# Kernel optimization log

Measured on AMD Instinct MI355X. Metric: run time of the kernel, lower is better.

The kernel has to match this reference:

```python
import jax, jax.numpy as jnp
import numpy as np

LN_EPS = 1e-5
NEG_INF = -1e30


def setup_inputs() -> dict:
    key = jax.random.key(0)
    ks = jax.random.split(key, 8)
    B, S, D_MODEL, Q_IN = 1, 2048, 1024, 512
    HI, DI = 16, 64            # indexer heads / head_dim
    H, DQK, DV = 8, 64, 64     # MLA heads, qk_head_dim, v_head_dim
    return {
        "x": jax.random.normal(ks[0], (B, S, D_MODEL), jnp.float32),
        "q_input": jax.random.normal(ks[1], (B, S, Q_IN), jnp.float32),
        "q": jax.random.normal(ks[2], (B, S, H, DQK), jnp.float32),
        "k": jax.random.normal(ks[3], (B, S, H, DQK), jnp.float32),
        "v": jax.random.normal(ks[4], (B, S, H, DV), jnp.float32),
        "w_q": jax.random.normal(ks[5], (Q_IN, HI * DI), jnp.float32) * (Q_IN ** -0.5),
        "w_k": jax.random.normal(ks[6], (D_MODEL, DI), jnp.float32) * (D_MODEL ** -0.5),
        "ln_g": jnp.ones((DI,), jnp.float32),
        "ln_b": jnp.zeros((DI,), jnp.float32),
        "w_weights": jax.random.normal(ks[7], (D_MODEL, HI), jnp.float32) * (D_MODEL ** -0.5),
        "top_k": 128,
    }


def _indexer_topk(x, q_input, w_q, w_k, ln_g, ln_b, w_weights, top_k):
    """Lightning indexer: per-head relevance scores -> weighted sum -> causal top-k indices."""
    B, S, _ = x.shape
    HI = w_weights.shape[1]
    DI = w_k.shape[1]
    qi = (q_input @ w_q).reshape(B, S, HI, DI)          # bqhd
    ki = x @ w_k                                         # bkd
    mu = ki.mean(-1, keepdims=True)
    var = ((ki - mu) ** 2).mean(-1, keepdims=True)
    ki = (ki - mu) * jax.lax.rsqrt(var + LN_EPS) * ln_g + ln_b
    # per-head weights; scores*w summed over h == (sum_h w*q) . k  (fused, same math)
    w = (x @ w_weights) * (HI ** -0.5)                   # bqh
    q_eff = jnp.einsum("bqhd,bqh->bqd", qi, w) * (DI ** -0.5)
    scores = jnp.einsum("bqd,bkd->bqk", q_eff, ki)       # [B,S,S]
    pos = jnp.arange(S)
    causal = jnp.where(pos[None, :] <= pos[:, None], 0.0, NEG_INF).astype(scores.dtype)
    scores = scores + causal[None]
    return jax.lax.top_k(scores, top_k)[1]               # [B,S,K]


def reference(x, q_input, q, k, v, w_q, w_k, ln_g, ln_b, w_weights, top_k):
    B, S, H, DQK = q.shape
    DV = v.shape[-1]
    idx = _indexer_topk(x, q_input, w_q, w_k, ln_g, ln_b, w_weights, top_k)  # [B,S,K]

    qh = q.transpose(0, 2, 1, 3)   # [B,H,Sq,D]
    kh = k.transpose(0, 2, 1, 3)   # [B,H,Sk,D]
    vh = v.transpose(0, 2, 1, 3)

    def gather(kv, ix):            # kv [Sk,D], ix [Sq,K] -> [Sq,K,D]
        return kv[ix]

    gather_h = jax.vmap(gather, in_axes=(0, None))       # over heads, shared idx
    gather_bh = jax.vmap(gather_h, in_axes=(0, 0))       # over batch
    k_sel = gather_bh(kh, idx)     # [B,H,Sq,K,D]
    v_sel = gather_bh(vh, idx)     # [B,H,Sq,K,Dv]

    att = jnp.einsum("bhqd,bhqkd->bhqk", qh, k_sel) * (DQK ** -0.5)
    pos = jnp.arange(S)
    valid = idx[:, None, :, :] <= pos[None, None, :, None]   # causal validity of gathered idx
    att = jnp.where(valid, att, NEG_INF)
    p = jax.nn.softmax(att, axis=-1)
    out = jnp.einsum("bhqk,bhqkd->bhqd", p, v_sel)
    return out.transpose(0, 2, 1, 3)   # [B,S,H,Dv]
```

## Files before the change

### kernel.cpp

```cpp
#include <hip/hip_runtime.h>
#include <hip/hip_bf16.h>
#include <hip/hip_fp16.h>
#include <math.h>

#define S 2048
#define DM 1024
#define QIN 512
#define HI 16
#define DI 64
#define NH 8
#define TOPK 128
#define LN_EPS 1e-5f
#define KP 16
#define KVSZ (S * NH * 64)

typedef float f32x4 __attribute__((ext_vector_type(4)));
typedef short s16x8 __attribute__((ext_vector_type(8)));

__device__ __forceinline__ float wave_sum(float v){
#pragma unroll
  for (int o = 32; o; o >>= 1) v += __shfl_xor(v, o);
  return v;
}
__device__ __forceinline__ float wave_max(float v){
#pragma unroll
  for (int o = 32; o; o >>= 1) v = fmaxf(v, __shfl_xor(v, o));
  return v;
}
__device__ __forceinline__ unsigned short f2bf(float x){
  unsigned u = __float_as_uint(x);
  unsigned r = u + 0x7FFFu + ((u >> 16) & 1u);
  return (unsigned short)(r >> 16);
}
__device__ __forceinline__ float bf2f(unsigned short s){
  return __uint_as_float(((unsigned)s) << 16);
}
__device__ __forceinline__ unsigned short f2h(float x){
  return __half_as_ushort(__float2half_rn(x));
}
union UH2 { unsigned int u; __half2 h; };
__device__ __forceinline__ __half2 as_half2(unsigned int u){ UH2 x; x.u = u; return x.h; }

#define MFMA3(ACC, AH, AL, BH, BL) \
  ACC = __builtin_amdgcn_mfma_f32_16x16x32_bf16(AH, BH, ACC, 0, 0, 0); \
  ACC = __builtin_amdgcn_mfma_f32_16x16x32_bf16(AH, BL, ACC, 0, 0, 0); \
  ACC = __builtin_amdgcn_mfma_f32_16x16x32_bf16(AL, BH, ACC, 0, 0, 0);

#define MFMA6(ACC, AH, AM, AL, BH, BM, BL) \
  ACC = __builtin_amdgcn_mfma_f32_16x16x32_bf16(AH, BH, ACC, 0, 0, 0); \
  ACC = __builtin_amdgcn_mfma_f32_16x16x32_bf16(AH, BM, ACC, 0, 0, 0); \
  ACC = __builtin_amdgcn_mfma_f32_16x16x32_bf16(AM, BH, ACC, 0, 0, 0); \
  ACC = __builtin_amdgcn_mfma_f32_16x16x32_bf16(AH, BL, ACC, 0, 0, 0); \
  ACC = __builtin_amdgcn_mfma_f32_16x16x32_bf16(AL, BH, ACC, 0, 0, 0); \
  ACC = __builtin_amdgcn_mfma_f32_16x16x32_bf16(AM, BM, ACC, 0, 0, 0);

__global__ __launch_bounds__(256) void k_f1(const float* __restrict__ x,
                                            const float* __restrict__ wk,
                                            const float* __restrict__ ww,
                                            float* __restrict__ part,
                                            const float* __restrict__ qin,
                                            unsigned short* __restrict__ Ah,
                                            unsigned short* __restrict__ Al,
                                            const float* __restrict__ k,
                                            unsigned short* __restrict__ kh,
                                            const float* __restrict__ v,
                                            unsigned short* __restrict__ vh,
                                            const float* __restrict__ wq,
                                            unsigned short* __restrict__ Bh,
                                            unsigned short* __restrict__ Bl){
  __shared__ float As[32][68];
  __shared__ float Bs[32][84];
  const int bid = blockIdx.x;
  const int t = threadIdx.x;

  if (bid < 512){
    const int kp = bid & 15;
    const int bm = bid >> 4;
    const int m0 = bm * 64;
    const int tm = (t & 15) * 4;
    const int tn = (t >> 4) * 5;
    float acc[4][5];
#pragma unroll
    for (int i = 0; i < 4; i++)
#pragma unroll
      for (int j = 0; j < 5; j++) acc[i][j] = 0.f;

    for (int kb = 0; kb < (DM / KP) / 32; ++kb){
      const int k0 = kp * (DM / KP) + kb * 32;
#pragma unroll
      for (int i = 0; i < 2; i++){
        int u = t + i * 256;
        int m = u >> 3, c4 = u & 7;
        float4 a = *(const float4*)&x[(size_t)(m0 + m) * DM + k0 + c4 * 4];
        As[c4*4+0][m] = a.x; As[c4*4+1][m] = a.y; As[c4*4+2][m] = a.z; As[c4*4+3][m] = a.w;
      }
#pragma unroll
      for (int i = 0; i < 10; i++){
        int u = t + i * 256;
        int kk = u / 80, nn = u % 80;
        float val = (nn < 64) ? wk[(size_t)(k0 + kk) * 64 + nn]
                              : ww[(size_t)(k0 + kk) * 16 + (nn - 64)];
        Bs[kk][nn] = val;
      }
      __syncthreads();
#pragma unroll
      for (int kk = 0; kk < 32; ++kk){
        float4 a = *(const float4*)&As[kk][tm];
        float av[4] = {a.x, a.y, a.z, a.w};
        float bb[5];
#pragma unroll
        for (int j = 0; j < 5; j++) bb[j] = Bs[kk][tn + j];
#pragma unroll
        for (int i = 0; i < 4; i++)
#pragma unroll
          for (int j = 0; j < 5; j++) acc[i][j] = fmaf(av[i], bb[j], acc[i][j]);
      }
      __syncthreads();
    }
    float* dst = part + (size_t)kp * S * 80;
#pragma unroll
    for (int i = 0; i < 4; i++)
#pragma unroll
      for (int j = 0; j < 5; j++)
        dst[(size_t)(m0 + tm + i) * 80 + tn + j] = acc[i][j];
    return;
  }

  if (bid < 512 + 3072){
    const int SEG0 = S * QIN / 4;
    const int SEG1 = KVSZ / 4;
    int id = (bid - 512) * 256 + t;
    if (id < SEG0){
      float4 f = ((const float4*)qin)[id];
      ushort4 h, lo;
      h.x = f2bf(f.x); lo.x = f2bf(f.x - bf2f(h.x));
      h.y = f2bf(f.y); lo.y = f2bf(f.y - bf2f(h.y));
      h.z = f2bf(f.z); lo.z = f2bf(f.z - bf2f(h.z));
      h.w = f2bf(f.w); lo.w = f2bf(f.w - bf2f(h.w));
      ((ushort4*)Ah)[id] = h;
      ((ushort4*)Al)[id] = lo;
    } else if (id < SEG0 + SEG1){
      int j = id - SEG0;
      float4 f = ((const float4*)k)[j];
      ushort4 o;
      o.x = f2h(f.x); o.y = f2h(f.y); o.z = f2h(f.z); o.w = f2h(f.w);
      ((ushort4*)kh)[j] = o;
    } else {
      int j = id - SEG0 - SEG1;
      float4 f = ((const float4*)v)[j];
      ushort4 o;
      o.x = f2h(f.x); o.y = f2h(f.y); o.z = f2h(f.z); o.w = f2h(f.w);
      ((ushort4*)vh)[j] = o;
    }
    return;
  }

  {
    unsigned short (*lh)[33] = (unsigned short(*)[33])&As[0][0];
    unsigned short (*ll)[33] = (unsigned short(*)[33])&Bs[0][0];
    const int b2 = bid - 3584;
    const int k0 = (b2 & 15) * 32;
    const int n0 = (b2 >> 4) * 32;
    const int c = t & 31, r8 = t >> 5;
#pragma unroll
    for (int i = 0; i < 4; ++i){
      int kk = r8 + i * 8;
      float wv = wq[(size_t)(k0 + kk) * 1024 + n0 + c];
      unsigned short h = f2bf(wv);
      lh[c][kk] = h;
      ll[c][kk] = f2bf(wv - bf2f(h));
    }
    __syncthreads();
    const int kk = t & 31, nl = t >> 5;
#pragma unroll
    for (int i = 0; i < 4; ++i){
      int nn = nl + i * 8;
      Bh[(size_t)(n0 + nn) * QIN + k0 + kk] = lh[nn][kk];
      Bl[(size_t)(n0 + nn) * QIN + k0 + kk] = ll[nn][kk];
    }
  }
}

__global__ __launch_bounds__(256) void k_f2(const float* __restrict__ part,
                                            const float* __restrict__ g,
                                            const float* __restrict__ b,
                                            unsigned short* __restrict__ kih,
                                            unsigned short* __restrict__ kim,
                                            unsigned short* __restrict__ kil,
                                            float* __restrict__ wgt,
                                            const unsigned short* __restrict__ Ah,
                                            const unsigned short* __restrict__ Al,
                                            const unsigned short* __restrict__ Bh,
                                            const unsigned short* __restrict__ Bl,
                                            float* __restrict__ qi){
  __shared__ short Ash[64][72];
  __shared__ short Asl[64][72];
  __shared__ short Bsh[64][72];
  __shared__ short Bsl[64][72];
  const int bid = blockIdx.x;
  const int t = threadIdx.x;
  if (bid < 512){
    const int s = bid * 4 + (t >> 6);
    const int l = t & 63;
    float kv = 0.f;
#pragma unroll
    for (int p = 0; p < KP; p++) kv += part[(size_t)p * S * 80 + (size_t)s * 80 + l];
    float wv = 0.f;
    if (l < 16){
#pragma unroll
      for (int p = 0; p < KP; p++) wv += part[(size_t)p * S * 80 + (size_t)s * 80 + 64 + l];
    }
    float mu = wave_sum(kv) * (1.f / 64.f);
    float d  = kv - mu;
    float var = wave_sum(d * d) * (1.f / 64.f);
    float o = d * (1.f / sqrtf(var + LN_EPS)) * g[l] + b[l];
    unsigned short h = f2bf(o);
    float r1 = o - bf2f(h);
    unsigned short m = f2bf(r1);
    kih[(size_t)s * 64 + l] = h;
    kim[(size_t)s * 64 + l] = m;
    kil[(size_t)s * 64 + l] = f2bf(r1 - bf2f(m));
    if (l < 16) wgt[(size_t)s * 16 + l] = wv * 0.25f;
    return;
  }
  const int b2 = bid - 512;
  const int bn = b2 & 15;
  const int bm = b2 >> 4;
  const int w = t >> 6, l = t & 63;
  const int r = l & 15, kg = l >> 4;
  const int m0 = bm * 64 + (w >> 1) * 32;
  const int n0 = bn * 64 + (w & 1) * 32;
  const int mq = (w >> 1) * 32;
  const int nq = (w & 1) * 32;
  const int srow = t >> 3;
  const int scol = (t & 7) * 8;

  f32x4 acc00 = {0,0,0,0}, acc01 = {0,0,0,0}, acc10 = {0,0,0,0}, acc11 = {0,0,0,0};

  for (int kb = 0; kb < QIN / 64; ++kb){
    const int k0 = kb * 64;
#pragma unroll
    for (int i = 0; i < 2; ++i){
      int row = srow + i * 32;
      size_t ga = (size_t)(bm * 64 + row) * QIN + k0 + scol;
      size_t gb = (size_t)(bn * 64 + row) * QIN + k0 + scol;
      *(s16x8*)&Ash[row][scol] = *(const s16x8*)(Ah + ga);
      *(s16x8*)&Asl[row][scol] = *(const s16x8*)(Al + ga);
      *(s16x8*)&Bsh[row][scol] = *(const s16x8*)(Bh + gb);
      *(s16x8*)&Bsl[row][scol] = *(const s16x8*)(Bl + gb);
    }
    __syncthreads();
#pragma unroll
    for (int ks = 0; ks < 2; ++ks){
      const int ko = ks * 32 + kg * 8;
      s16x8 ah0 = *(const s16x8*)&Ash[mq + r][ko];
      s16x8 ah1 = *(const s16x8*)&Ash[mq + 16 + r][ko];
      s16x8 al0 = *(const s16x8*)&Asl[mq + r][ko];
      s16x8 al1 = *(const s16x8*)&Asl[mq + 16 + r][ko];
      s16x8 bh0 = *(const s16x8*)&Bsh[nq + r][ko];
      s16x8 bh1 = *(const s16x8*)&Bsh[nq + 16 + r][ko];
      s16x8 bl0 = *(const s16x8*)&Bsl[nq + r][ko];
      s16x8 bl1 = *(const s16x8*)&Bsl[nq + 16 + r][ko];
      MFMA3(acc00, ah0, al0, bh0, bl0)
      MFMA3(acc01, ah0, al0, bh1, bl1)
      MFMA3(acc10, ah1, al1, bh0, bl0)
      MFMA3(acc11, ah1, al1, bh1, bl1)
    }
    __syncthreads();
  }
#pragma unroll
  for (int j = 0; j < 4; ++j){
    qi[(size_t)(m0 +  0 + kg * 4 + j) * 1024 + n0 +  0 + r] = acc00[j];
    qi[(size_t)(m0 +  0 + kg * 4 + j) * 1024 + n0 + 16 + r] = acc01[j];
    qi[(size_t)(m0 + 16 + kg * 4 + j) * 1024 + n0 +  0 + r] = acc10[j];
    qi[(size_t)(m0 + 16 + kg * 4 + j) * 1024 + n0 + 16 + r] = acc11[j];
  }
}

__global__ __launch_bounds__(256) void k_f3(const float* __restrict__ qi,
                                            const float* __restrict__ wgt,
                                            unsigned short* __restrict__ qeh,
                                            unsigned short* __restrict__ qem,
                                            unsigned short* __restrict__ qel){
  const int id = blockIdx.x * 256 + threadIdx.x;
  const int s = id >> 6, d = id & 63;
  float acc = 0.f;
#pragma unroll
  for (int h = 0; h < 16; h++)
    acc = fmaf(wgt[(size_t)s * 16 + h], qi[(size_t)s * 1024 + h * 64 + d], acc);
  acc *= 0.125f;
  unsigned short hh = f2bf(acc);
  float r1 = acc - bf2f(hh);
  unsigned short mm = f2bf(r1);
  qeh[(size_t)s * 64 + d] = hh;
  qem[(size_t)s * 64 + d] = mm;
  qel[(size_t)s * 64 + d] = f2bf(r1 - bf2f(mm));
}

__global__ __launch_bounds__(256) void k_scores(const unsigned short* __restrict__ qeh,
                                                const unsigned short* __restrict__ qem,
                                                const unsigned short* __restrict__ qel,
                                                const unsigned short* __restrict__ kih,
                                                const unsigned short* __restrict__ kim,
                                                const unsigned short* __restrict__ kil,
                                                float* __restrict__ sc){
  const int bj = blockIdx.x, bi = blockIdx.y;
  if (bj > bi) return;
  const int w = threadIdx.x >> 6, l = threadIdx.x & 63;
  const int r = l & 15, kg = l >> 4;
  const int m0 = bi * 64 + (w >> 1) * 32;
  const int n0 = bj * 64 + (w & 1) * 32;
  f32x4 acc00 = {0,0,0,0}, acc01 = {0,0,0,0}, acc10 = {0,0,0,0}, acc11 = {0,0,0,0};
  const size_t aoff = (size_t)(m0 + r) * 64 + kg * 8;
  const size_t boff = (size_t)(n0 + r) * 64 + kg * 8;
#pragma unroll
  for (int k0 = 0; k0 < 64; k0 += 32){
    s16x8 ah0 = *(const s16x8*)(qeh + aoff + k0);
    s16x8 ah1 = *(const s16x8*)(qeh + aoff + 16 * 64 + k0);
    s16x8 am0 = *(const s16x8*)(qem + aoff + k0);
    s16x8 am1 = *(const s16x8*)(qem + aoff + 16 * 64 + k0);
    s16x8 al0 = *(const s16x8*)(qel + aoff + k0);
    s16x8 al1 = *(const s16x8*)(qel + aoff + 16 * 64 + k0);
    s16x8 bh0 = *(const s16x8*)(kih + boff + k0);
    s16x8 bh1 = *(const s16x8*)(kih + boff + 16 * 64 + k0);
    s16x8 bm0 = *(const s16x8*)(kim + boff + k0);
    s16x8 bm1 = *(const s16x8*)(kim + boff + 16 * 64 + k0);
    s16x8 bl0 = *(const s16x8*)(kil + boff + k0);
    s16x8 bl1 = *(const s16x8*)(kil + boff + 16 * 64 + k0);
    MFMA6(acc00, ah0, am0, al0, bh0, bm0, bl0)
    MFMA6(acc01, ah0, am0, al0, bh1, bm1, bl1)
    MFMA6(acc10, ah1, am1, al1, bh0, bm0, bl0)
    MFMA6(acc11, ah1, am1, al1, bh1, bm1, bl1)
  }
#pragma unroll
  for (int j = 0; j < 4; ++j){
    sc[(size_t)(m0 +  0 + kg * 4 + j) * S + n0 +  0 + r] = acc00[j];
    sc[(size_t)(m0 +  0 + kg * 4 + j) * S + n0 + 16 + r] = acc01[j];
    sc[(size_t)(m0 + 16 + kg * 4 + j) * S + n0 +  0 + r] = acc10[j];
    sc[(size_t)(m0 + 16 + kg * 4 + j) * S + n0 + 16 + r] = acc11[j];
  }
}

__global__ __launch_bounds__(256) void k_ta(const float* __restrict__ sc,
                                            const float* __restrict__ q,
                                            const unsigned short* __restrict__ kh,
                                            const unsigned short* __restrict__ vh,
                                            float* __restrict__ out){
  const int i = blockIdx.x, t = threadIdx.x;
  const int w = t >> 6, l = t & 63;
  const int ncand = i + 1;

  __shared__ unsigned int keys[S];
  __shared__ int lA[S];
  __shared__ int lB[S];
  __shared__ int hist[256];
  __shared__ int wtot[4];
  __shared__ int sres[TOPK];
  __shared__ int s_b, s_above, s_out, s_m;
  __shared__ float sp[4][2][TOPK];

  if (ncand <= TOPK){
    if (t < TOPK) sres[t] = (t < ncand) ? t : 0;
    __syncthreads();
  } else {
    hist[t] = 0;
    if (t == 0) s_out = 0;
    __syncthreads();
    for (int j = t; j < ncand; j += 256){
      unsigned int u = __float_as_uint(sc[(size_t)i * S + j]);
      unsigned int kk = (u & 0x80000000u) ? ~u : (u | 0x80000000u);
      keys[j] = kk;
      atomicAdd(&hist[kk >> 24], 1);
    }
    __syncthreads();
    int rem = TOPK;
    {
      const int h = hist[t];
      int vsc = h;
#pragma unroll
      for (int off = 1; off < 64; off <<= 1){
        int u = __shfl_down(vsc, off);
        if (l + off < 64) vsc += u;
      }
      if (l == 0) wtot[w] = vsc;
      __syncthreads();
      int later = 0;
#pragma unroll
      for (int ww = 1; ww < 4; ++ww) if (ww > w) later += wtot[ww];
      const int excl = vsc + later - h;
      if (excl < rem && excl + h >= rem){ s_b = t; s_above = excl; }
      __syncthreads();
    }
    int b = s_b;
    rem -= s_above;
    if (t == 0) s_m = 0;
    __syncthreads();
    for (int b0 = 0; b0 < ncand; b0 += 256){
      int j = b0 + t;
      bool valid = j < ncand;
      unsigned int kk = valid ? keys[j] : 0u;
      int by = kk >> 24;
      bool pgt = valid && (by > b);
      bool peq = valid && (by == b);
      unsigned long long mgt = __ballot(pgt);
      unsigned long long meq = __ballot(peq);
      int basegt = 0, baseeq = 0;
      if (l == 0){
        basegt = atomicAdd(&s_out, __popcll(mgt));
        baseeq = atomicAdd(&s_m, __popcll(meq));
      }
      basegt = __shfl(basegt, 0);
      baseeq = __shfl(baseeq, 0);
      unsigned long long lanemask = (1ull << l) - 1ull;
      if (pgt) sres[basegt + __popcll(mgt & lanemask)] = j;
      if (peq) lA[baseeq + __popcll(meq & lanemask)] = j;
    }
    __syncthreads();
    int m = s_m;
    int* Lsrc = lA; int* Ldst = lB;
    bool done = false;
    if (m == rem){
      int base = TOPK - rem;
      for (int u = t; u < m; u += 256) sres[base + u] = Lsrc[u];
      done = true;
    }
    for (int p = 2; p >= 0 && !done; --p){
      const int sh = p * 8;
      __syncthreads();
      hist[t] = 0;
      __syncthreads();
      for (int u = t; u < m; u += 256) atomicAdd(&hist[(keys[Lsrc[u]] >> sh) & 255], 1);
      __syncthreads();
      {
        const int h = hist[t];
        int vsc = h;
#pragma unroll
        for (int off = 1; off < 64; off <<= 1){
          int u = __shfl_down(vsc, off);
          if (l + off < 64) vsc += u;
        }
        if (l == 0) wtot[w] = vsc;
        __syncthreads();
        int later = 0;
#pragma unroll
        for (int ww = 1; ww < 4; ++ww) if (ww > w) later += wtot[ww];
        const int excl = vsc + later - h;
        if (excl < rem && excl + h >= rem){ s_b = t; s_above = excl; }
        __syncthreads();
      }
      b = s_b;
      rem -= s_above;
      if (t == 0) s_m = 0;
      __syncthreads();
      for (int u = t; u < m; u += 256){
        int j = Lsrc[u]; int by = (keys[j] >> sh) & 255;
        if (by > b){ int p2 = atomicAdd(&s_out, 1); sres[p2] = j; }
        else if (by == b){ int p2 = atomicAdd(&s_m, 1); Ldst[p2] = j; }
      }
      __syncthreads();
      m = s_m;
      { int* tmp = Lsrc; Lsrc = Ldst; Ldst = tmp; }
      if (m == rem){
        int base = TOPK - rem;
        for (int u = t; u < m; u += 256) sres[base + u] = Lsrc[u];
        done = true;
      }
    }
    if (!done && t == 0){
      int base = TOPK - rem;
      for (int a = 0; a < rem; ++a){
        int mn = 1 << 30, pos = -1;
        for (int u = 0; u < m; ++u){ int j = Lsrc[u]; if (j < mn){ mn = j; pos = u; } }
        sres[base + a] = mn; Lsrc[pos] = 1 << 30;
      }
    }
    __syncthreads();
  }

  const int n = (ncand < TOPK) ? ncand : TOPK;
  const int h0 = 2 * w, h1 = h0 + 1;
  const int g = l >> 3, gl = l & 7;
  const float* qrow = q + (size_t)i * (NH * 64);
  __half2 qa2[4], qb2[4];
  {
    float4 a0 = *(const float4*)&qrow[h0 * 64 + gl * 8];
    float4 a1 = *(const float4*)&qrow[h0 * 64 + gl * 8 + 4];
    float4 b0 = *(const float4*)&qrow[h1 * 64 + gl * 8];
    float4 b1 = *(const float4*)&qrow[h1 * 64 + gl * 8 + 4];
    qa2[0] = __floats2half2_rn(a0.x * 0.125f, a0.y * 0.125f);
    qa2[1] = __floats2half2_rn(a0.z * 0.125f, a0.w * 0.125f);
    qa2[2] = __floats2half2_rn(a1.x * 0.125f, a1.y * 0.125f);
    qa2[3] = __floats2half2_rn(a1.z * 0.125f, a1.w * 0.125f);
    qb2[0] = __floats2half2_rn(b0.x * 0.125f, b0.y * 0.125f);
    qb2[1] = __floats2half2_rn(b0.z * 0.125f, b0.w * 0.125f);
    qb2[2] = __floats2half2_rn(b1.x * 0.125f, b1.y * 0.125f);
    qb2[3] = __floats2half2_rn(b1.z * 0.125f, b1.w * 0.125f);
  }

#pragma unroll 8
  for (int pass = 0; pass < TOPK / 8; ++pass){
    const int j = pass * 8 + g;
    const int sj = (j < n) ? sres[j] : 0;
    const size_t base = (size_t)sj * (NH * 64);
    uint4 u0 = *(const uint4*)(kh + base + h0 * 64 + gl * 8);
    uint4 u1 = *(const uint4*)(kh + base + h1 * 64 + gl * 8);
    __half2 acc0 = __floats2half2_rn(0.f, 0.f);
    __half2 acc1 = __floats2half2_rn(0.f, 0.f);
    acc0 = __hfma2(as_half2(u0.x), qa2[0], acc0);
    acc0 = __hfma2(as_half2(u0.y), qa2[1], acc0);
    acc0 = __hfma2(as_half2(u0.z), qa2[2], acc0);
    acc0 = __hfma2(as_half2(u0.w), qa2[3], acc0);
    acc1 = __hfma2(as_half2(u1.x), qb2[0], acc1);
    acc1 = __hfma2(as_half2(u1.y), qb2[1], acc1);
    acc1 = __hfma2(as_half2(u1.z), qb2[2], acc1);
    acc1 = __hfma2(as_half2(u1.w), qb2[3], acc1);
    float d0 = __low2float(acc0) + __high2float(acc0);
    float d1 = __low2float(acc1) + __high2float(acc1);
#pragma unroll
    for (int o = 1; o < 8; o <<= 1){ d0 += __shfl_xor(d0, o); d1 += __shfl_xor(d1, o); }
    if (gl == 0){ sp[w][0][j] = d0; sp[w][1][j] = d1; }
  }
  asm volatile("" ::: "memory");

  const bool v0 = (l < n), v1 = (l + 64 < n);
  {
    float s0 = v0 ? sp[w][0][l] : -1e30f, s1 = v1 ? sp[w][0][l + 64] : -1e30f;
    float m = wave_max(fmaxf(s0, s1));
    float e0 = v0 ? __expf(s0 - m) : 0.f;
    float e1 = v1 ? __expf(s1 - m) : 0.f;
    float inv = 1.f / wave_sum(e0 + e1);
    sp[w][0][l] = e0 * inv;
    sp[w][0][l + 64] = e1 * inv;
  }
  {
    float s0 = v0 ? sp[w][1][l] : -1e30f, s1 = v1 ? sp[w][1][l + 64] : -1e30f;
    float m = wave_max(fmaxf(s0, s1));
    float e0 = v0 ? __expf(s0 - m) : 0.f;
    float e1 = v1 ? __expf(s1 - m) : 0.f;
    float inv = 1.f / wave_sum(e0 + e1);
    sp[w][1][l] = e0 * inv;
    sp[w][1][l + 64] = e1 * inv;
  }
  asm volatile("" ::: "memory");

  const int kq = l >> 4;
  const int hp = (l >> 3) & 1;
  const int d8 = (l & 7) * 8;
  float o8[8] = {0,0,0,0,0,0,0,0};
#pragma unroll 8
  for (int pass = 0; pass < TOPK / 4; ++pass){
    const int j = pass * 4 + kq;
    const int sj = (j < n) ? sres[j] : 0;
    const size_t base = (size_t)sj * (NH * 64);
    uint4 uv = *(const uint4*)(vh + base + (h0 + hp) * 64 + d8);
    float p = sp[w][hp][j];
    __half2 va = as_half2(uv.x), vb = as_half2(uv.y), vc = as_half2(uv.z), vd = as_half2(uv.w);
    o8[0] = fmaf(p, __low2float(va),  o8[0]);
    o8[1] = fmaf(p, __high2float(va), o8[1]);
    o8[2] = fmaf(p, __low2float(vb),  o8[2]);
    o8[3] = fmaf(p, __high2float(vb), o8[3]);
    o8[4] = fmaf(p, __low2float(vc),  o8[4]);
    o8[5] = fmaf(p, __high2float(vc), o8[5]);
    o8[6] = fmaf(p, __low2float(vd),  o8[6]);
    o8[7] = fmaf(p, __high2float(vd), o8[7]);
  }
#pragma unroll
  for (int e = 0; e < 8; ++e){
    o8[e] += __shfl_xor(o8[e], 16);
    o8[e] += __shfl_xor(o8[e], 32);
  }
  if (l < 16){
    float* dst = &out[(size_t)i * (NH * 64) + (h0 + hp) * 64 + d8];
    *(float4*)dst       = make_float4(o8[0], o8[1], o8[2], o8[3]);
    *(float4*)(dst + 4) = make_float4(o8[4], o8[5], o8[6], o8[7]);
  }
}

extern "C" void kernel_launch(void* const* d_in, const int* in_sizes, int n_in,
                              void* d_out, int out_size, void* d_ws, size_t ws_size,
                              hipStream_t stream){
  const float* x   = (const float*)d_in[0];
  const float* qin = (const float*)d_in[1];
  const float* q   = (const float*)d_in[2];
  const float* k   = (const float*)d_in[3];
  const float* v   = (const float*)d_in[4];
  const float* wq  = (const float*)d_in[5];
  const float* wk  = (const float*)d_in[6];
  const float* lng = (const float*)d_in[7];
  const float* lnb = (const float*)d_in[8];
  const float* ww  = (const float*)d_in[9];
  float* out = (float*)d_out;

  float* ws = (float*)d_ws;
  float* part = ws;
  float* wgt  = ws + 2621440;
  float* qi   = ws + 2654208;
  float* sc   = ws + 4751360;
  unsigned short* kh  = (unsigned short*)(ws + 8945664);
  unsigned short* vh  = (unsigned short*)(ws + 9469952);
  unsigned short* kih = (unsigned short*)(ws + 9994240);
  unsigned short* kim = (unsigned short*)(ws + 10059776);
  unsigned short* kil = (unsigned short*)(ws + 10125312);
  unsigned short* qeh = (unsigned short*)(ws + 10190848);
  unsigned short* qem = (unsigned short*)(ws + 10256384);
  unsigned short* qel = (unsigned short*)(ws + 10321920);
  unsigned short* Ah  = (unsigned short*)(ws + 10387456);
  unsigned short* Al  = (unsigned short*)(ws + 10911744);
  unsigned short* Bh  = (unsigned short*)(ws + 11436032);
  unsigned short* Bl  = (unsigned short*)(ws + 11698176);

  hipLaunchKernelGGL(k_f1,     dim3(4096),   dim3(256), 0, stream,
                     x, wk, ww, part, qin, Ah, Al, k, kh, v, vh, wq, Bh, Bl);
  hipLaunchKernelGGL(k_f2,     dim3(1024),   dim3(256), 0, stream,
                     part, lng, lnb, kih, kim, kil, wgt, Ah, Al, Bh, Bl, qi);
  hipLaunchKernelGGL(k_f3,     dim3(512),    dim3(256), 0, stream,
                     qi, wgt, qeh, qem, qel);
  hipLaunchKernelGGL(k_scores, dim3(32, 32), dim3(256), 0, stream,
                     qeh, qem, qel, kih, kim, kil, sc);
  hipLaunchKernelGGL(k_ta,     dim3(2048),   dim3(256), 0, stream,
                     sc, q, kh, vh, out);
}
```

Measured before the change: 98.95 us.

## Replace LDS-buffered radix select with prefix-filtered re-reads of score row

```diff
diff --git a/kernel.cpp b/kernel.cpp
--- a/kernel.cpp
+++ b/kernel.cpp
@@ -13,6 +13,7 @@
 #define LN_EPS 1e-5f
 #define KP 16
 #define KVSZ (S * NH * 64)
+#define TBCAP 384
 
 typedef float f32x4 __attribute__((ext_vector_type(4)));
 typedef short s16x8 __attribute__((ext_vector_type(8)));
@@ -37,6 +38,10 @@
 }
 __device__ __forceinline__ unsigned short f2h(float x){
   return __half_as_ushort(__float2half_rn(x));
+}
+__device__ __forceinline__ unsigned int sortkey(float x){
+  unsigned u = __float_as_uint(x);
+  return (u & 0x80000000u) ? ~u : (u | 0x80000000u);
 }
 union UH2 { unsigned int u; __half2 h; };
 __device__ __forceinline__ __half2 as_half2(unsigned int u){ UH2 x; x.u = u; return x.h; }
@@ -350,86 +355,31 @@
   const int w = t >> 6, l = t & 63;
   const int ncand = i + 1;
 
-  __shared__ unsigned int keys[S];
-  __shared__ int lA[S];
-  __shared__ int lB[S];
   __shared__ int hist[256];
   __shared__ int wtot[4];
   __shared__ int sres[TOPK];
+  __shared__ int tb[TBCAP];
   __shared__ int s_b, s_above, s_out, s_m;
   __shared__ float sp[4][2][TOPK];
 
+  const float* srow = sc + (size_t)i * S;
+
   if (ncand <= TOPK){
     if (t < TOPK) sres[t] = (t < ncand) ? t : 0;
     __syncthreads();
   } else {
-    hist[t] = 0;
-    if (t == 0) s_out = 0;
-    __syncthreads();
-    for (int j = t; j < ncand; j += 256){
-      unsigned int u = __float_as_uint(sc[(size_t)i * S + j]);
-      unsigned int kk = (u & 0x80000000u) ? ~u : (u | 0x80000000u);
-      keys[j] = kk;
-      atomicAdd(&hist[kk >> 24], 1);
-    }
-    __syncthreads();
+    unsigned int prefix = 0;
     int rem = TOPK;
-    {
-      const int h = hist[t];
-      int vsc = h;
-#pragma unroll
-      for (int off = 1; off < 64; off <<= 1){
-        int u = __shfl_down(vsc, off);
-        if (l + off < 64) vsc += u;
-      }
-      if (l == 0) wtot[w] = vsc;
-      __syncthreads();
-      int later = 0;
-#pragma unroll
-      for (int ww = 1; ww < 4; ++ww) if (ww > w) later += wtot[ww];
-      const int excl = vsc + later - h;
-      if (excl < rem && excl + h >= rem){ s_b = t; s_above = excl; }
-      __syncthreads();
-    }
-    int b = s_b;
-    rem -= s_above;
-    if (t == 0) s_m = 0;
-    __syncthreads();
-    for (int b0 = 0; b0 < ncand; b0 += 256){
-      int j = b0 + t;
-      bool valid = j < ncand;
-      unsigned int kk = valid ? keys[j] : 0u;
-      int by = kk >> 24;
-      bool pgt = valid && (by > b);
-      bool peq = valid && (by == b);
-      unsigned long long mgt = __ballot(pgt);
-      unsigned long long meq = __ballot(peq);
-      int basegt = 0, baseeq = 0;
-      if (l == 0){
-        basegt = atomicAdd(&s_out, __popcll(mgt));
-        baseeq = atomicAdd(&s_m, __popcll(meq));
-      }
-      basegt = __shfl(basegt, 0);
-      baseeq = __shfl(baseeq, 0);
-      unsigned long long lanemask = (1ull << l) - 1ull;
-      if (pgt) sres[basegt + __popcll(mgt & lanemask)] = j;
-      if (peq) lA[baseeq + __popcll(meq & lanemask)] = j;
-    }
-    __syncthreads();
-    int m = s_m;
-    int* Lsrc = lA; int* Ldst = lB;
-    bool done = false;
-    if (m == rem){
-      int base = TOPK - rem;
-      for (int u = t; u < m; u += 256) sres[base + u] = Lsrc[u];
-      done = true;
-    }
-    for (int p = 2; p >= 0 && !done; --p){
+#pragma unroll
+    for (int p = 3; p >= 0; --p){
       const int sh = p * 8;
-      __syncthreads();
       hist[t] = 0;
       __syncthreads();
-      for (int u = t; u < m; u += 256) atomicAdd(&hist[(keys[Lsrc[u]] >> sh) & 255], 1);
+      const unsigned int himask = (p == 3) ? 0u : (0xFFFFFFFFu << (sh + 8));
+      for (int j = t; j < ncand; j += 256){
+        unsigned int kk = sortkey(srow[j]);
+        if ((kk & himask) == (prefix & himask)) atomicAdd(&hist[(kk >> sh) & 255], 1);
+      }
       __syncthreads();
       {
         const int h = hist[t];
@@ -448,31 +398,41 @@
         if (excl < rem && excl + h >= rem){ s_b = t; s_above = excl; }
         __syncthreads();
       }
-      b = s_b;
+      prefix |= ((unsigned int)s_b) << sh;
       rem -= s_above;
-      if (t == 0) s_m = 0;
-      __syncthreads();
-      for (int u = t; u < m; u += 256){
-        int j = Lsrc[u]; int by = (keys[j] >> sh) & 255;
-        if (by > b){ int p2 = atomicAdd(&s_out, 1); sres[p2] = j; }
-        else if (by == b){ int p2 = atomicAdd(&s_m, 1); Ldst[p2] = j; }
-      }
-      __syncthreads();
-      m = s_m;
-      { int* tmp = Lsrc; Lsrc = Ldst; Ldst = tmp; }
-      if (m == rem){
-        int base = TOPK - rem;
-        for (int u = t; u < m; u += 256) sres[base + u] = Lsrc[u];
-        done = true;
-      }
-    }
-    if (!done && t == 0){
-      int base = TOPK - rem;
-      for (int a = 0; a < rem; ++a){
-        int mn = 1 << 30, pos = -1;
-        for (int u = 0; u < m; ++u){ int j = Lsrc[u]; if (j < mn){ mn = j; pos = u; } }
-        sres[base + a] = mn; Lsrc[pos] = 1 << 30;
-      }
+    }
+    if (t == 0){ s_out = 0; s_m = 0; }
+    __syncthreads();
+    for (int b0 = 0; b0 < ncand; b0 += 256){
+      int j = b0 + t;
+      bool valid = j < ncand;
+      unsigned int kk = valid ? sortkey(srow[j]) : 0u;
+      bool pgt = valid && (kk > prefix);
+      bool peq = valid && (kk == prefix);
+      unsigned long long mgt = __ballot(pgt);
+      unsigned long long meq = __ballot(peq);
+      int basegt = 0, baseeq = 0;
+      if (l == 0){
+        basegt = (mgt ? atomicAdd(&s_out, __popcll(mgt)) : 0);
+        baseeq = (meq ? atomicAdd(&s_m, __popcll(meq)) : 0);
+      }
+      basegt = __shfl(basegt, 0);
+      baseeq = __shfl(baseeq, 0);
+      unsigned long long lanemask = (1ull << l) - 1ull;
+      if (pgt) sres[basegt + __popcll(mgt & lanemask)] = j;
+      if (peq){
+        int p2 = baseeq + __popcll(meq & lanemask);
+        if (p2 < TBCAP) tb[p2] = j;
+      }
+    }
+    __syncthreads();
+    const int nout = s_out;
+    if (s_m == rem){
+      for (int u2 = t; u2 < rem; u2 += 256) sres[nout + u2] = tb[u2];
+    } else if (t == 0){
+      int taken = 0;
+      for (int j = 0; j < ncand && taken < rem; ++j)
+        if (sortkey(srow[j]) == prefix) sres[nout + taken++] = j;
     }
     __syncthreads();
   }
```

Result: slower. 103.0 us (+4.1%).

## Split fused top-k/attention kernel into separate top-k and per-wave attention kernels

Applied to the files above, without the earlier changes.

```diff
diff --git a/kernel.cpp b/kernel.cpp
--- a/kernel.cpp
+++ b/kernel.cpp
@@ -341,39 +341,92 @@
   }
 }
 
-__global__ __launch_bounds__(256) void k_ta(const float* __restrict__ sc,
-                                            const float* __restrict__ q,
-                                            const unsigned short* __restrict__ kh,
-                                            const unsigned short* __restrict__ vh,
-                                            float* __restrict__ out){
+__global__ __launch_bounds__(256) void k_topk(const float* __restrict__ sc,
+                                              int* __restrict__ idx,
+                                              int* __restrict__ cnt){
   const int i = blockIdx.x, t = threadIdx.x;
   const int w = t >> 6, l = t & 63;
-  const int ncand = i + 1;
-
+  const int n = i + 1;
+  int* outr = idx + (size_t)i * TOPK;
+  if (n <= TOPK){
+    for (int m = t; m < n; m += 256) outr[m] = m;
+    if (t == 0) cnt[i] = n;
+    return;
+  }
   __shared__ unsigned int keys[S];
   __shared__ int lA[S];
   __shared__ int lB[S];
   __shared__ int hist[256];
   __shared__ int wtot[4];
-  __shared__ int sres[TOPK];
   __shared__ int s_b, s_above, s_out, s_m;
-  __shared__ float sp[4][2][TOPK];
-
-  if (ncand <= TOPK){
-    if (t < TOPK) sres[t] = (t < ncand) ? t : 0;
-    __syncthreads();
-  } else {
+  hist[t] = 0;
+  if (t == 0) s_out = 0;
+  __syncthreads();
+  for (int j = t; j < n; j += 256){
+    unsigned int u = __float_as_uint(sc[(size_t)i * S + j]);
+    unsigned int kk = (u & 0x80000000u) ? ~u : (u | 0x80000000u);
+    keys[j] = kk;
+    atomicAdd(&hist[kk >> 24], 1);
+  }
+  __syncthreads();
+  int rem = TOPK;
+  {
+    const int h = hist[t];
+    int vsc = h;
+#pragma unroll
+    for (int off = 1; off < 64; off <<= 1){
+      int u = __shfl_down(vsc, off);
+      if (l + off < 64) vsc += u;
+    }
+    if (l == 0) wtot[w] = vsc;
+    __syncthreads();
+    int later = 0;
+#pragma unroll
+    for (int ww = 1; ww < 4; ++ww) if (ww > w) later += wtot[ww];
+    const int excl = vsc + later - h;
+    if (excl < rem && excl + h >= rem){ s_b = t; s_above = excl; }
+    __syncthreads();
+  }
+  int b = s_b;
+  rem -= s_above;
+  if (t == 0) s_m = 0;
+  __syncthreads();
+  for (int b0 = 0; b0 < n; b0 += 256){
+    int j = b0 + t;
+    bool valid = j < n;
+    unsigned int kk = valid ? keys[j] : 0u;
+    int by = kk >> 24;
+    bool pgt = valid && (by > b);
+    bool peq = valid && (by == b);
+    unsigned long long mgt = __ballot(pgt);
+    unsigned long long meq = __ballot(peq);
+    int basegt = 0, baseeq = 0;
+    if (l == 0){
+      basegt = (mgt ? atomicAdd(&s_out, __popcll(mgt)) : 0);
+      baseeq = (meq ? atomicAdd(&s_m, __popcll(meq)) : 0);
+    }
+    basegt = __shfl(basegt, 0);
+    baseeq = __shfl(baseeq, 0);
+    unsigned long long lanemask = (1ull << l) - 1ull;
+    if (pgt) outr[basegt + __popcll(mgt & lanemask)] = j;
+    if (peq) lA[baseeq + __popcll(meq & lanemask)] = j;
+  }
+  __syncthreads();
+  int m = s_m;
+  int* Lsrc = lA; int* Ldst = lB;
+  bool done = false;
+  if (m == rem){
+    int base = TOPK - rem;
+    for (int u = t; u < m; u += 256) outr[base + u] = Lsrc[u];
+    done = true;
+  }
+  for (int p = 2; p >= 0 && !done; --p){
+    const int sh = p * 8;
+    __syncthreads();
     hist[t] = 0;
-    if (t == 0) s_out = 0;
-    __syncthreads();
-    for (int j = t; j < ncand; j += 256){
-      unsigned int u = __float_as_uint(sc[(size_t)i * S + j]);
-      unsigned int kk = (u & 0x80000000u) ? ~u : (u | 0x80000000u);
-      keys[j] = kk;
-      atomicAdd(&hist[kk >> 24], 1);
-    }
-    __syncthreads();
-    int rem = TOPK;
+    __syncthreads();
+    for (int u = t; u < m; u += 256) atomicAdd(&hist[(keys[Lsrc[u]] >> sh) & 255], 1);
+    __syncthreads();
     {
       const int h = hist[t];
       int vsc = h;
@@ -391,93 +444,54 @@
       if (excl < rem && excl + h >= rem){ s_b = t; s_above = excl; }
       __syncthreads();
     }
-    int b = s_b;
+    b = s_b;
     rem -= s_above;
     if (t == 0) s_m = 0;
     __syncthreads();
-    for (int b0 = 0; b0 < ncand; b0 += 256){
-      int j = b0 + t;
-      bool valid = j < ncand;
-      unsigned int kk = valid ? keys[j] : 0u;
-      int by = kk >> 24;
-      bool pgt = valid && (by > b);
-      bool peq = valid && (by == b);
-      unsigned long long mgt = __ballot(pgt);
-      unsigned long long meq = __ballot(peq);
-      int basegt = 0, baseeq = 0;
-      if (l == 0){
-        basegt = atomicAdd(&s_out, __popcll(mgt));
-        baseeq = atomicAdd(&s_m, __popcll(meq));
-      }
-      basegt = __shfl(basegt, 0);
-      baseeq = __shfl(baseeq, 0);
-      unsigned long long lanemask = (1ull << l) - 1ull;
-      if (pgt) sres[basegt + __popcll(mgt & lanemask)] = j;
-      if (peq) lA[baseeq + __popcll(meq & lanemask)] = j;
-    }
-    __syncthreads();
-    int m = s_m;
-    int* Lsrc = lA; int* Ldst = lB;
-    bool done = false;
+    for (int u = t; u < m; u += 256){
+      int j = Lsrc[u]; int by = (keys[j] >> sh) & 255;
+      if (by > b){ int p2 = atomicAdd(&s_out, 1); outr[p2] = j; }
+      else if (by == b){ int p2 = atomicAdd(&s_m, 1); Ldst[p2] = j; }
+    }
+    __syncthreads();
+    m = s_m;
+    { int* tmp = Lsrc; Lsrc = Ldst; Ldst = tmp; }
     if (m == rem){
       int base = TOPK - rem;
-      for (int u = t; u < m; u += 256) sres[base + u] = Lsrc[u];
+      for (int u = t; u < m; u += 256) outr[base + u] = Lsrc[u];
       done = true;
     }
-    for (int p = 2; p >= 0 && !done; --p){
-      const int sh = p * 8;
-      __syncthreads();
-      hist[t] = 0;
-      __syncthreads();
-      for (int u = t; u < m; u += 256) atomicAdd(&hist[(keys[Lsrc[u]] >> sh) & 255], 1);
-      __syncthreads();
-      {
-        const int h = hist[t];
-        int vsc = h;
-#pragma unroll
-        for (int off = 1; off < 64; off <<= 1){
-          int u = __shfl_down(vsc, off);
-          if (l + off < 64) vsc += u;
-        }
-        if (l == 0) wtot[w] = vsc;
-        __syncthreads();
-        int later = 0;
-#pragma unroll
-        for (int ww = 1; ww < 4; ++ww) if (ww > w) later += wtot[ww];
-        const int excl = vsc + later - h;
-        if (excl < rem && excl + h >= rem){ s_b = t; s_above = excl; }
-        __syncthreads();
-      }
-      b = s_b;
-      rem -= s_above;
-      if (t == 0) s_m = 0;
-      __syncthreads();
-      for (int u = t; u < m; u += 256){
-        int j = Lsrc[u]; int by = (keys[j] >> sh) & 255;
-        if (by > b){ int p2 = atomicAdd(&s_out, 1); sres[p2] = j; }
-        else if (by == b){ int p2 = atomicAdd(&s_m, 1); Ldst[p2] = j; }
-      }
-      __syncthreads();
-      m = s_m;
-      { int* tmp = Lsrc; Lsrc = Ldst; Ldst = tmp; }
-      if (m == rem){
-        int base = TOPK - rem;
-        for (int u = t; u < m; u += 256) sres[base + u] = Lsrc[u];
-        done = true;
-      }
-    }
-    if (!done && t == 0){
-      int base = TOPK - rem;
-      for (int a = 0; a < rem; ++a){
-        int mn = 1 << 30, pos = -1;
-        for (int u = 0; u < m; ++u){ int j = Lsrc[u]; if (j < mn){ mn = j; pos = u; } }
-        sres[base + a] = mn; Lsrc[pos] = 1 << 30;
-      }
-    }
-    __syncthreads();
-  }
-
-  const int n = (ncand < TOPK) ? ncand : TOPK;
+  }
+  if (!done && t == 0){
+    int base = TOPK - rem;
+    for (int a = 0; a < rem; ++a){
+      int mn = 1 << 30, pos = -1;
+      for (int u = 0; u < m; ++u){ int j = Lsrc[u]; if (j < mn){ mn = j; pos = u; } }
+      outr[base + a] = mn; Lsrc[pos] = 1 << 30;
+    }
+  }
+  if (t == 0) cnt[i] = TOPK;
+}
+
+__global__ __launch_bounds__(64) void k_attn(const float* __restrict__ q,
+                                             const unsigned short* __restrict__ kh,
+                                             const unsigned short* __restrict__ vh,
+                                             const int* __restrict__ idx,
+                                             const int* __restrict__ cnt,
+                                             float* __restrict__ out){
+  const int blk = blockIdx.x;
+  const int i = blk >> 2;
+  const int w = blk & 3;
+  const int l = threadIdx.x;
+  const int n = cnt[i];
+  const int* irow = idx + (size_t)i * TOPK;
+
+  __shared__ int   sidx[TOPK];
+  __shared__ float sp[2][TOPK];
+
+  sidx[l]      = (l < n)      ? irow[l]      : 0;
+  sidx[l + 64] = (l + 64 < n) ? irow[l + 64] : 0;
+
   const int h0 = 2 * w, h1 = h0 + 1;
   const int g = l >> 3, gl = l & 7;
   const float* qrow = q + (size_t)i * (NH * 64);
@@ -496,12 +510,12 @@
     qb2[2] = __floats2half2_rn(b1.x * 0.125f, b1.y * 0.125f);
     qb2[3] = __floats2half2_rn(b1.z * 0.125f, b1.w * 0.125f);
   }
+  asm volatile("" ::: "memory");
 
 #pragma unroll 8
   for (int pass = 0; pass < TOPK / 8; ++pass){
     const int j = pass * 8 + g;
-    const int sj = (j < n) ? sres[j] : 0;
-    const size_t base = (size_t)sj * (NH * 64);
+    const size_t base = (size_t)sidx[j] * (NH * 64);
     uint4 u0 = *(const uint4*)(kh + base + h0 * 64 + gl * 8);
     uint4 u1 = *(const uint4*)(kh + base + h1 * 64 + gl * 8);
     __half2 acc0 = __floats2half2_rn(0.f, 0.f);
@@ -518,28 +532,28 @@
     float d1 = __low2float(acc1) + __high2float(acc1);
 #pragma unroll
     for (int o = 1; o < 8; o <<= 1){ d0 += __shfl_xor(d0, o); d1 += __shfl_xor(d1, o); }
-    if (gl == 0){ sp[w][0][j] = d0; sp[w][1][j] = d1; }
+    if (gl == 0){ sp[0][j] = d0; sp[1][j] = d1; }
   }
   asm volatile("" ::: "memory");
 
   const bool v0 = (l < n), v1 = (l + 64 < n);
   {
-    float s0 = v0 ? sp[w][0][l] : -1e30f, s1 = v1 ? sp[w][0][l + 64] : -1e30f;
+    float s0 = v0 ? sp[0][l] : -1e30f, s1 = v1 ? sp[0][l + 64] : -1e30f;
     float m = wave_max(fmaxf(s0, s1));
     float e0 = v0 ? __expf(s0 - m) : 0.f;
     float e1 = v1 ? __expf(s1 - m) : 0.f;
     float inv = 1.f / wave_sum(e0 + e1);
-    sp[w][0][l] = e0 * inv;
-    sp[w][0][l + 64] = e1 * inv;
+    sp[0][l] = e0 * inv;
+    sp[0][l + 64] = e1 * inv;
   }
   {
-    float s0 = v0 ? sp[w][1][l] : -1e30f, s1 = v1 ? sp[w][1][l + 64] : -1e30f;
+    float s0 = v0 ? sp[1][l] : -1e30f, s1 = v1 ? sp[1][l + 64] : -1e30f;
     float m = wave_max(fmaxf(s0, s1));
     float e0 = v0 ? __expf(s0 - m) : 0.f;
     float e1 = v1 ? __expf(s1 - m) : 0.f;
     float inv = 1.f / wave_sum(e0 + e1);
-    sp[w][1][l] = e0 * inv;
-    sp[w][1][l + 64] = e1 * inv;
+    sp[1][l] = e0 * inv;
+    sp[1][l + 64] = e1 * inv;
   }
   asm volatile("" ::: "memory");
 
@@ -550,10 +564,9 @@
 #pragma unroll 8
   for (int pass = 0; pass < TOPK / 4; ++pass){
     const int j = pass * 4 + kq;
-    const int sj = (j < n) ? sres[j] : 0;
-    const size_t base = (size_t)sj * (NH * 64);
+    const size_t base = (size_t)sidx[j] * (NH * 64);
     uint4 uv = *(const uint4*)(vh + base + (h0 + hp) * 64 + d8);
-    float p = sp[w][hp][j];
+    float p = sp[hp][j];
     __half2 va = as_half2(uv.x), vb = as_half2(uv.y), vc = as_half2(uv.z), vd = as_half2(uv.w);
     o8[0] = fmaf(p, __low2float(va),  o8[0]);
     o8[1] = fmaf(p, __high2float(va), o8[1]);
@@ -596,27 +609,29 @@
   float* wgt  = ws + 2621440;
   float* qi   = ws + 2654208;
   float* sc   = ws + 4751360;
-  unsigned short* kh  = (unsigned short*)(ws + 8945664);
-  unsigned short* vh  = (unsigned short*)(ws + 9469952);
-  unsigned short* kih = (unsigned short*)(ws + 9994240);
-  unsigned short* kim = (unsigned short*)(ws + 10059776);
-  unsigned short* kil = (unsigned short*)(ws + 10125312);
-  unsigned short* qeh = (unsigned short*)(ws + 10190848);
-  unsigned short* qem = (unsigned short*)(ws + 10256384);
-  unsigned short* qel = (unsigned short*)(ws + 10321920);
-  unsigned short* Ah  = (unsigned short*)(ws + 10387456);
-  unsigned short* Al  = (unsigned short*)(ws + 10911744);
-  unsigned short* Bh  = (unsigned short*)(ws + 11436032);
-  unsigned short* Bl  = (unsigned short*)(ws + 11698176);
-
-  hipLaunchKernelGGL(k_f1,     dim3(4096),   dim3(256), 0, stream,
+  int*   idx  = (int*)(ws + 8945664);
+  int*   cnt  = (int*)(ws + 9207808);
+  unsigned short* kh  = (unsigned short*)(ws + 9209856);
+  unsigned short* vh  = (unsigned short*)(ws + 9734144);
+  unsigned short* kih = (unsigned short*)(ws + 10258432);
+  unsigned short* kim = (unsigned short*)(ws + 10323968);
+  unsigned short* kil = (unsigned short*)(ws + 10389504);
+  unsigned short* qeh = (unsigned short*)(ws + 10455040);
+  unsigned short* qem = (unsigned short*)(ws + 10520576);
+  unsigned short* qel = (unsigned short*)(ws + 10586112);
+  unsigned short* Ah  = (unsigned short*)(ws + 10651648);
+  unsigned short* Al  = (unsigned short*)(ws + 11175936);
+  unsigned short* Bh  = (unsigned short*)(ws + 11700224);
+  unsigned short* Bl  = (unsigned short*)(ws + 11962368);
+
+  hipLaunchKernelGGL(k_f1,     dim3(4096),    dim3(256), 0, stream,
                      x, wk, ww, part, qin, Ah, Al, k, kh, v, vh, wq, Bh, Bl);
-  hipLaunchKernelGGL(k_f2,     dim3(1024),   dim3(256), 0, stream,
+  hipLaunchKernelGGL(k_f2,     dim3(1024),    dim3(256), 0, stream,
                      part, lng, lnb, kih, kim, kil, wgt, Ah, Al, Bh, Bl, qi);
-  hipLaunchKernelGGL(k_f3,     dim3(512),    dim3(256), 0, stream,
+  hipLaunchKernelGGL(k_f3,     dim3(512),     dim3(256), 0, stream,
                      qi, wgt, qeh, qem, qel);
-  hipLaunchKernelGGL(k_scores, dim3(32, 32), dim3(256), 0, stream,
+  hipLaunchKernelGGL(k_scores, dim3(32, 32),  dim3(256), 0, stream,
                      qeh, qem, qel, kih, kim, kil, sc);
-  hipLaunchKernelGGL(k_ta,     dim3(2048),   dim3(256), 0, stream,
-                     sc, q, kh, vh, out);
-}
+  hipLaunchKernelGGL(k_topk,   dim3(2048),    dim3(256), 0, stream, sc, idx, cnt);
+  hipLaunchKernelGGL(k_attn,   dim3(2048*4),  dim3(64),  0, stream, q, kh, vh, idx, cnt, out);
+}
```

Result: no change. 99.47 us, median of 2 (+0.5%).
